# Optimization experiments

Hardware: AMD Instinct MI355X
Metric: run time of the kernel (lower is better)

Reference implementation:

```python
import jax, jax.numpy as jnp
import numpy as np

E, T_MAX, H, L, V = 384, 256, 6, 6, 65
DH = E // H  # 64
EPS = 1e-5


def setup_inputs() -> dict:
    key = jax.random.key(0)
    ks = jax.random.split(key, 24)
    B, T = 128, 256
    s = 0.02
    inp = {
        "input_indices": jax.random.randint(ks[0], (B, T), 0, V, dtype=jnp.int64) if jax.config.read("jax_enable_x64") else jax.random.randint(ks[0], (B, T), 0, V, dtype=jnp.int32),
        "targets": jax.random.randint(ks[1], (B, T), 0, V, dtype=jnp.int32),
        "tok_emb": s * jax.random.normal(ks[2], (V, E), jnp.float32),
        "pos_emb": s * jax.random.normal(ks[3], (T_MAX, E), jnp.float32),
        "Wq": s * jax.random.normal(ks[4], (L, H, E, DH), jnp.float32),
        "Wk": s * jax.random.normal(ks[5], (L, H, E, DH), jnp.float32),
        "Wv": s * jax.random.normal(ks[6], (L, H, E, DH), jnp.float32),
        "Wo": s * jax.random.normal(ks[7], (L, E, E), jnp.float32),
        "bo": jnp.zeros((L, E), jnp.float32),
        "ln1_s": jnp.ones((L, E), jnp.float32),
        "ln1_b": jnp.zeros((L, E), jnp.float32),
        "ln2_s": jnp.ones((L, E), jnp.float32),
        "ln2_b": jnp.zeros((L, E), jnp.float32),
        "W1": s * jax.random.normal(ks[8], (L, E, 4 * E), jnp.float32),
        "b1": jnp.zeros((L, 4 * E), jnp.float32),
        "W2": s * jax.random.normal(ks[9], (L, 4 * E, E), jnp.float32),
        "b2": jnp.zeros((L, E), jnp.float32),
        "lnf_s": jnp.ones((E,), jnp.float32),
        "lnf_b": jnp.zeros((E,), jnp.float32),
        "Wout": s * jax.random.normal(ks[10], (E, V), jnp.float32),
        "bout": jnp.zeros((V,), jnp.float32),
    }
    return inp


def _ln(x, s, b):
    m = x.mean(-1, keepdims=True)
    v = ((x - m) ** 2).mean(-1, keepdims=True)
    return (x - m) * jax.lax.rsqrt(v + EPS) * s + b


def _forward(input_indices, targets, tok_emb, pos_emb, Wq, Wk, Wv, Wo, bo,
             ln1_s, ln1_b, ln2_s, ln2_b, W1, b1, W2, b2, lnf_s, lnf_b, Wout, bout):
    B, T = input_indices.shape
    x = tok_emb[input_indices] + pos_emb[:T]  # [B,T,E]
    causal = jnp.tril(jnp.ones((T, T), bool))
    scale = DH ** -0.5

    def block(x, p):
        wq, wk, wv, wo, bo_, l1s, l1b, l2s, l2b, w1, b1_, w2, b2_ = p
        h = _ln(x, l1s, l1b)
        q = jnp.einsum("bte,hed->bhtd", h, wq)
        k = jnp.einsum("bte,hed->bhtd", h, wk)
        v = jnp.einsum("bte,hed->bhtd", h, wv)
        scores = jnp.einsum("bhtd,bhsd->bhts", q, k) * scale
        scores = jnp.where(causal, scores, -jnp.inf)
        w = jax.nn.softmax(scores, axis=-1)
        att = jnp.einsum("bhts,bhsd->bhtd", w, v)  # [B,H,T,DH]
        att = att.transpose(0, 2, 1, 3).reshape(B, T, E)  # concat heads
        x = x + att @ wo + bo_
        h2 = _ln(x, l2s, l2b)
        ff = jax.nn.relu(h2 @ w1 + b1_) @ w2 + b2_
        return x + ff, None

    x, _ = jax.lax.scan(block, x, (Wq, Wk, Wv, Wo, bo, ln1_s, ln1_b, ln2_s, ln2_b, W1, b1, W2, b2))
    x = _ln(x, lnf_s, lnf_b)
    logits = x @ Wout + bout  # [B,T,V]
    logp = jax.nn.log_softmax(logits, axis=-1)
    nll = -jnp.take_along_axis(logp, targets[..., None], axis=-1)[..., 0]
    loss = nll.mean()
    return logits, loss


def reference(input_indices, targets, tok_emb, pos_emb, Wq, Wk, Wv, Wo, bo,
              ln1_s, ln1_b, ln2_s, ln2_b, W1, b1, W2, b2, lnf_s, lnf_b, Wout, bout):
    return _forward(input_indices, targets, tok_emb, pos_emb, Wq, Wk, Wv, Wo, bo,
                    ln1_s, ln1_b, ln2_s, ln2_b, W1, b1, W2, b2, lnf_s, lnf_b, Wout, bout)
```

## Files before the change

kernel.cpp:

```cpp
#include <hip/hip_runtime.h>

#define BT      32768
#define T_SEQ   256
#define E_DIM   384
#define NH      6
#define NL      6
#define VOC     65
#define FF_DIM  1536
#define QKV_N   1152

typedef short bf16x8 __attribute__((ext_vector_type(8)));
typedef float f32x4  __attribute__((ext_vector_type(4)));
typedef unsigned short u16;

typedef const unsigned int __attribute__((address_space(1))) gu32;
typedef unsigned int       __attribute__((address_space(3))) lu32;

__device__ __forceinline__ u16 f2bf(float x) {
  unsigned u = __builtin_bit_cast(unsigned, x);
  u += 0x7fffu + ((u >> 16) & 1u);
  return (u16)(u >> 16);
}
__device__ __forceinline__ float bf2f(u16 v) {
  unsigned u = ((unsigned)v) << 16;
  return __builtin_bit_cast(float, u);
}

__device__ __forceinline__ void load_lds_16(const void* g, void* l) {
  __builtin_amdgcn_global_load_lds((gu32*)g, (lu32*)l, 16, 0, 0);
}

__global__ __launch_bounds__(256) void transpose_t(
    const float* __restrict__ src, u16* __restrict__ dst, int R, int C,
    long sbs, long dbs_outer, int inner, long dbs_inner, long dbase) {
  __shared__ float t[32][33];
  const int b = blockIdx.z;
  const float* s = src + (long)b * sbs;
  u16* d = dst + dbase + (long)(b / inner) * dbs_outer + (long)(b % inner) * dbs_inner;
  const int r0 = blockIdx.x * 32, c0 = blockIdx.y * 32;
  const int tx = threadIdx.x & 31, ty = threadIdx.x >> 5;
#pragma unroll
  for (int i = 0; i < 4; i++) {
    int rr = ty + i * 8;
    int r = r0 + rr, c = c0 + tx;
    if (r < R && c < C) t[rr][tx] = s[(long)r * C + c];
  }
  __syncthreads();
#pragma unroll
  for (int i = 0; i < 4; i++) {
    int cc = ty + i * 8;
    int c = c0 + cc, r = r0 + tx;
    if (c < C && r < R) d[(long)c * R + r] = f2bf(t[tx][cc]);
  }
}

__global__ __launch_bounds__(256) void embed_k(const int* __restrict__ idx,
                                               const float* __restrict__ tok,
                                               const float* __restrict__ pos,
                                               u16* __restrict__ x) {
  int i = blockIdx.x * 256 + threadIdx.x;
  int bt = i / 48, q = i - bt * 48;
  int t = bt & 255;
  const float4* tp = (const float4*)(tok + (size_t)idx[bt] * E_DIM + q * 8);
  const float4* pp = (const float4*)(pos + (size_t)t * E_DIM + q * 8);
  float4 a0 = tp[0], a1 = tp[1], p0 = pp[0], p1 = pp[1];
  u16 o[8];
  o[0] = f2bf(a0.x + p0.x); o[1] = f2bf(a0.y + p0.y);
  o[2] = f2bf(a0.z + p0.z); o[3] = f2bf(a0.w + p0.w);
  o[4] = f2bf(a1.x + p1.x); o[5] = f2bf(a1.y + p1.y);
  o[6] = f2bf(a1.z + p1.z); o[7] = f2bf(a1.w + p1.w);
  *(bf16x8*)(x + (size_t)bt * E_DIM + q * 8) = *(bf16x8*)o;
}

__global__ __launch_bounds__(256) void ln_k(const u16* __restrict__ x,
                                            const float* __restrict__ gam,
                                            const float* __restrict__ bet,
                                            u16* __restrict__ out) {
  int tid = threadIdx.x, lane = tid & 63, w = tid >> 6;
  size_t token = (size_t)blockIdx.x * 4 + w;
  const u16* xr = x + token * E_DIM;
  u16 raw[6];
  *(uint2*)raw          = *(const uint2*)(xr + 4 * lane);
  *(unsigned*)(raw + 4) = *(const unsigned*)(xr + 256 + 2 * lane);
  float v[6]; float s = 0.f;
#pragma unroll
  for (int i = 0; i < 6; i++) { v[i] = bf2f(raw[i]); s += v[i]; }
#pragma unroll
  for (int d = 1; d < 64; d <<= 1) s += __shfl_xor(s, d);
  float mean = s * (1.f / E_DIM);
  float q = 0.f;
#pragma unroll
  for (int i = 0; i < 6; i++) { float d0 = v[i] - mean; q += d0 * d0; }
#pragma unroll
  for (int d = 1; d < 64; d <<= 1) q += __shfl_xor(q, d);
  float r = rsqrtf(q * (1.f / E_DIM) + 1e-5f);
  int e[6] = {4 * lane, 4 * lane + 1, 4 * lane + 2, 4 * lane + 3,
              256 + 2 * lane, 256 + 2 * lane + 1};
  u16 o[6];
#pragma unroll
  for (int i = 0; i < 6; i++)
    o[i] = f2bf((v[i] - mean) * r * gam[e[i]] + bet[e[i]]);
  u16* orow = out + token * E_DIM;
  *(uint2*)(orow + 4 * lane)          = *(uint2*)o;
  *(unsigned*)(orow + 256 + 2 * lane) = *(unsigned*)(o + 4);
}

__global__ __launch_bounds__(256) void gemm_d(
    const u16* __restrict__ A, const u16* __restrict__ Bt, int K, int Nstore,
    const float* __restrict__ bias, const u16* __restrict__ resid,
    u16* __restrict__ outH, float* __restrict__ outF, int relu) {
  __shared__ u16 smem[16384];
  u16* As = smem;
  u16* Bs = smem + 8192;
  const int tid = threadIdx.x, lane = tid & 63, wv = tid >> 6;
  const int quad = lane >> 4, l16 = lane & 15;
  const int m0 = blockIdx.x * 128, n0 = blockIdx.y * 128;
  const int wm = (wv & 1) * 64, wn = (wv >> 1) * 64;

  const int lrow = lane >> 2;
  const int lchunk = (lane & 3) ^ ((lane >> 3) & 3);

  f32x4 acc[4][4];
#pragma unroll
  for (int i = 0; i < 4; i++)
#pragma unroll
    for (int j = 0; j < 4; j++) acc[i][j] = (f32x4){0.f, 0.f, 0.f, 0.f};

  auto stage = [&](int sel, int k0) {
#pragma unroll
    for (int j = 0; j < 2; j++) {
      int rid = wv * 2 + j;
      int r = rid * 16 + lrow;
      load_lds_16(A + (size_t)(m0 + r) * K + k0 + lchunk * 8, &As[sel * 4096 + rid * 512]);
      load_lds_16(Bt + (size_t)(n0 + r) * K + k0 + lchunk * 8, &Bs[sel * 4096 + rid * 512]);
    }
  };

  const int NK = K >> 5;
  stage(0, 0);
  __syncthreads();
  const int slot = (quad ^ ((l16 >> 1) & 3)) * 8;
  for (int kt = 0; kt < NK; kt++) {
    const int cur = kt & 1;
    if (kt + 1 < NK) stage(cur ^ 1, (kt + 1) * 32);
    const u16* Ab = As + cur * 4096;
    const u16* Bb = Bs + cur * 4096;
    bf16x8 af[4], bfr[4];
#pragma unroll
    for (int i = 0; i < 4; i++) af[i]  = *(const bf16x8*)&Ab[(wm + i * 16 + l16) * 32 + slot];
#pragma unroll
    for (int j = 0; j < 4; j++) bfr[j] = *(const bf16x8*)&Bb[(wn + j * 16 + l16) * 32 + slot];
#pragma unroll
    for (int i = 0; i < 4; i++)
#pragma unroll
      for (int j = 0; j < 4; j++)
        acc[i][j] = __builtin_amdgcn_mfma_f32_16x16x32_bf16(af[i], bfr[j], acc[i][j], 0, 0, 0);
    __syncthreads();
  }

  if (outH) {
#pragma unroll
    for (int p = 0; p < 4; p++) {
      if (p) __syncthreads();
      if ((wv >> 1) == (p >> 1)) {
#pragma unroll
        for (int jj = 0; jj < 2; jj++) {
          int j = (p & 1) * 2 + jj;
          int gn = n0 + wn + j * 16 + l16;
          float bv = bias ? bias[gn] : 0.f;
          int lcol = jj * 16 + l16;
#pragma unroll
          for (int i = 0; i < 4; i++)
#pragma unroll
            for (int r = 0; r < 4; r++) {
              float v = acc[i][j][r] + bv;
              if (relu) v = fmaxf(v, 0.f);
              smem[(wm + i * 16 + quad * 4 + r) * 36 + lcol] = f2bf(v);
            }
        }
      }
      __syncthreads();
      const int gc0 = n0 + p * 32;
#pragma unroll
      for (int s = 0; s < 4; s++) {
        int row = s * 32 + (tid >> 3);
        int seg = (tid & 7) * 4;
        u16 pk[4];
        *(uint2*)pk = *(const uint2*)&smem[row * 36 + seg];
        size_t o = (size_t)(m0 + row) * Nstore + gc0 + seg;
        if (resid) {
          u16 rv[4];
          *(uint2*)rv = *(const uint2*)&resid[o];
#pragma unroll
          for (int q2 = 0; q2 < 4; q2++) pk[q2] = f2bf(bf2f(pk[q2]) + bf2f(rv[q2]));
        }
        *(uint2*)&outH[o] = *(uint2*)pk;
      }
    }
  } else {
#pragma unroll
    for (int j = 0; j < 4; j++) {
      const int gn = n0 + wn + j * 16 + l16;
      if (gn < Nstore) {
        const float bv = bias ? bias[gn] : 0.f;
#pragma unroll
        for (int i = 0; i < 4; i++)
#pragma unroll
          for (int r = 0; r < 4; r++) {
            const int gm = m0 + wm + i * 16 + quad * 4 + r;
            outF[(size_t)gm * Nstore + gn] = acc[i][j][r] + bv;
          }
      }
    }
  }
}

__global__ __launch_bounds__(512) void attn_k(const u16* __restrict__ qkv,
                                              u16* __restrict__ att) {
  __shared__ u16 Kc[64 * 64];
  __shared__ u16 Vtc[64 * 64];
  __shared__ u16 Pl[8 * 16 * 64];
  const int b = blockIdx.x / NH, h = blockIdx.x % NH;
  const int tid = threadIdx.x, lane = tid & 63, w = tid >> 6;
  const int quad = lane >> 4, l16 = lane & 15;
  const int rowb = b * T_SEQ;
  const int tiles[2] = {w, 15 - w};

  bf16x8 qf[2][2];
#pragma unroll
  for (int ti = 0; ti < 2; ti++)
#pragma unroll
    for (int kk = 0; kk < 2; kk++)
      qf[ti][kk] = *(const bf16x8*)(qkv + (size_t)(rowb + tiles[ti] * 16 + l16) * QKV_N +
                                    h * 64 + kk * 32 + quad * 8);

  f32x4 Oa[2][4];
  float mrun[2][4], lrun[2][4];
#pragma unroll
  for (int ti = 0; ti < 2; ti++) {
#pragma unroll
    for (int di = 0; di < 4; di++) Oa[ti][di] = (f32x4){0.f, 0.f, 0.f, 0.f};
#pragma unroll
    for (int r = 0; r < 4; r++) { mrun[ti][r] = -1e30f; lrun[ti][r] = 0.f; }
  }

  u16* Pw = &Pl[w * 1024];
  const int sr = tid >> 3, sseg = tid & 7;
  const int kst = sseg ^ (sr & 7) ^ ((sr >> 3) & 7);

  for (int c = 0; c < 4; c++) {
    const int s0 = c * 64;
    __syncthreads();
    *(uint4*)&Kc[sr * 64 + kst * 8] =
        *(const uint4*)(qkv + (size_t)(rowb + s0 + sr) * QKV_N + 384 + h * 64 + sseg * 8);
    {
      union { uint4 u; u16 us[8]; } tb;
      tb.u = *(const uint4*)(qkv + (size_t)(rowb + s0 + sr) * QKV_N + 768 + h * 64 + sseg * 8);
#pragma unroll
      for (int j = 0; j < 8; j++) {
        int d = sseg * 8 + j;
        int vst = (sr >> 3) ^ (d & 7) ^ ((d >> 3) & 7);
        Vtc[d * 64 + vst * 8 + (sr & 7)] = tb.us[j];
      }
    }
    __syncthreads();

    bf16x8 kf[4][2], vf[4][2];
    bool loaded = false;
#pragma unroll
    for (int ti = 0; ti < 2; ti++) {
      const int t = tiles[ti];
      if (t < 4 * c) continue;
      if (!loaded) {
        loaded = true;
#pragma unroll
        for (int ni = 0; ni < 4; ni++)
#pragma unroll
          for (int kk = 0; kk < 2; kk++) {
            int srow = ni * 16 + l16;
            int ks = (kk * 4 + quad) ^ (srow & 7) ^ ((srow >> 3) & 7);
            kf[ni][kk] = *(const bf16x8*)&Kc[srow * 64 + ks * 8];
            int drow = ni * 16 + l16;
            int vs = (kk * 4 + quad) ^ (drow & 7) ^ ((drow >> 3) & 7);
            vf[ni][kk] = *(const bf16x8*)&Vtc[drow * 64 + vs * 8];
          }
      }
      f32x4 S[4];
#pragma unroll
      for (int ni = 0; ni < 4; ni++) {
        f32x4 z = (f32x4){0.f, 0.f, 0.f, 0.f};
        z = __builtin_amdgcn_mfma_f32_16x16x32_bf16(qf[ti][0], kf[ni][0], z, 0, 0, 0);
        S[ni] = __builtin_amdgcn_mfma_f32_16x16x32_bf16(qf[ti][1], kf[ni][1], z, 0, 0, 0);
      }
      const bool diag = ((t >> 2) == c);
#pragma unroll
      for (int ni = 0; ni < 4; ni++)
#pragma unroll
        for (int r = 0; r < 4; r++) {
          float xv = S[ni][r] * 0.125f;
          if (diag) {
            int trow = t * 16 + quad * 4 + r;
            int s = s0 + ni * 16 + l16;
            if (s > trow) xv = -1e30f;
          }
          S[ni][r] = xv;
        }
#pragma unroll
      for (int r = 0; r < 4; r++) {
        float mx = fmaxf(fmaxf(S[0][r], S[1][r]), fmaxf(S[2][r], S[3][r]));
        mx = fmaxf(mx, __shfl_xor(mx, 1));
        mx = fmaxf(mx, __shfl_xor(mx, 2));
        mx = fmaxf(mx, __shfl_xor(mx, 4));
        mx = fmaxf(mx, __shfl_xor(mx, 8));
        float mnew = fmaxf(mrun[ti][r], mx);
        float alpha = __expf(mrun[ti][r] - mnew);
        float ls = 0.f;
#pragma unroll
        for (int ni = 0; ni < 4; ni++) {
          float p = __expf(S[ni][r] - mnew);
          S[ni][r] = p; ls += p;
        }
        ls += __shfl_xor(ls, 1); ls += __shfl_xor(ls, 2);
        ls += __shfl_xor(ls, 4); ls += __shfl_xor(ls, 8);
        lrun[ti][r] = lrun[ti][r] * alpha + ls;
        mrun[ti][r] = mnew;
#pragma unroll
        for (int di = 0; di < 4; di++) Oa[ti][di][r] *= alpha;
      }
#pragma unroll
      for (int ni = 0; ni < 4; ni++)
#pragma unroll
        for (int r = 0; r < 4; r++) {
          int ch = 2 * ni + (l16 >> 3);
          int st = ch ^ (quad | ((r & 1) << 2));
          Pw[(quad * 4 + r) * 64 + st * 8 + (l16 & 7)] = f2bf(S[ni][r]);
        }
      bf16x8 pf[2];
#pragma unroll
      for (int kk = 0; kk < 2; kk++) {
        int key = (l16 >> 2) | ((l16 & 1) << 2);
        int st = (kk * 4 + quad) ^ key;
        pf[kk] = *(const bf16x8*)&Pw[l16 * 64 + st * 8];
      }
#pragma unroll
      for (int di = 0; di < 4; di++) {
        Oa[ti][di] = __builtin_amdgcn_mfma_f32_16x16x32_bf16(pf[0], vf[di][0], Oa[ti][di], 0, 0, 0);
        Oa[ti][di] = __builtin_amdgcn_mfma_f32_16x16x32_bf16(pf[1], vf[di][1], Oa[ti][di], 0, 0, 0);
      }
    }
  }

#pragma unroll
  for (int ti = 0; ti < 2; ti++)
#pragma unroll
    for (int r = 0; r < 4; r++) {
      float inv = 1.f / lrun[ti][r];
      int trow = tiles[ti] * 16 + quad * 4 + r;
#pragma unroll
      for (int di = 0; di < 4; di++)
        att[(size_t)(rowb + trow) * E_DIM + h * 64 + di * 16 + l16] = f2bf(Oa[ti][di][r] * inv);
    }
}

__global__ __launch_bounds__(256) void loss_k(const float* __restrict__ logits,
                                              const int* __restrict__ tgt,
                                              float* __restrict__ loss) {
  __shared__ float part[4];
  const int tid = threadIdx.x, lane = tid & 63, w = tid >> 6;
  const int wave_id = blockIdx.x * 4 + w;
  float acc = 0.f;
  for (int t = wave_id; t < BT; t += 2048) {
    const float* row = logits + (size_t)t * VOC;
    float a = row[lane];
    float b = (lane == 0) ? row[64] : -1e30f;
    float mx = fmaxf(a, b);
#pragma unroll
    for (int d = 1; d < 64; d <<= 1) mx = fmaxf(mx, __shfl_xor(mx, d));
    float sum = __expf(a - mx) + ((lane == 0) ? __expf(b - mx) : 0.f);
#pragma unroll
    for (int d = 1; d < 64; d <<= 1) sum += __shfl_xor(sum, d);
    if (lane == 0) acc += mx + __logf(sum) - row[tgt[t]];
  }
  if (lane == 0) part[w] = acc;
  __syncthreads();
  if (tid == 0)
    atomicAdd(loss, (part[0] + part[1] + part[2] + part[3]) * (1.f / (float)BT));
}

extern "C" void kernel_launch(void* const* d_in, const int* in_sizes, int n_in,
                              void* d_out, int out_size, void* d_ws, size_t ws_size,
                              hipStream_t stream) {
  (void)in_sizes; (void)n_in; (void)out_size; (void)ws_size;
  const int*   idx  = (const int*)d_in[0];
  const int*   tgt  = (const int*)d_in[1];
  const float* tok  = (const float*)d_in[2];
  const float* pos  = (const float*)d_in[3];
  const float* Wq   = (const float*)d_in[4];
  const float* Wk   = (const float*)d_in[5];
  const float* Wv   = (const float*)d_in[6];
  const float* Wo   = (const float*)d_in[7];
  const float* bo   = (const float*)d_in[8];
  const float* ln1s = (const float*)d_in[9];
  const float* ln1b = (const float*)d_in[10];
  const float* ln2s = (const float*)d_in[11];
  const float* ln2b = (const float*)d_in[12];
  const float* W1   = (const float*)d_in[13];
  const float* b1   = (const float*)d_in[14];
  const float* W2   = (const float*)d_in[15];
  const float* b2   = (const float*)d_in[16];
  const float* lnfs = (const float*)d_in[17];
  const float* lnfb = (const float*)d_in[18];
  const float* Wout = (const float*)d_in[19];
  const float* bout = (const float*)d_in[20];

  char* w = (char*)d_ws;
  u16* x      = (u16*)w;    w += (size_t)BT * E_DIM * 2;
  u16* hb     = (u16*)w;    w += (size_t)BT * E_DIM * 2;
  u16* attb   = (u16*)w;    w += (size_t)BT * E_DIM * 2;
  u16* big    = (u16*)w;    w += (size_t)BT * FF_DIM * 2;
  u16* Wqkv_t = (u16*)w;    w += (size_t)NL * QKV_N * E_DIM * 2;
  u16* Wo_t   = (u16*)w;    w += (size_t)NL * E_DIM * E_DIM * 2;
  u16* W1_t   = (u16*)w;    w += (size_t)NL * FF_DIM * E_DIM * 2;
  u16* W2_t   = (u16*)w;    w += (size_t)NL * E_DIM * FF_DIM * 2;
  u16* Wout_t = (u16*)w;    w += (size_t)128 * E_DIM * 2;
  u16* qkv = big;
  u16* ff  = big;

  float* logits = (float*)d_out;
  float* loss   = logits + (size_t)BT * VOC;

  hipMemsetAsync(Wout_t, 0, 128 * E_DIM * 2, stream);
  transpose_t<<<dim3(12, 2, 36), 256, 0, stream>>>(Wq, Wqkv_t, 384, 64,
      24576, 442368, 6, 24576, 0);
  transpose_t<<<dim3(12, 2, 36), 256, 0, stream>>>(Wk, Wqkv_t, 384, 64,
      24576, 442368, 6, 24576, (long)384 * 384);
  transpose_t<<<dim3(12, 2, 36), 256, 0, stream>>>(Wv, Wqkv_t, 384, 64,
      24576, 442368, 6, 24576, (long)768 * 384);
  transpose_t<<<dim3(12, 12, 6), 256, 0, stream>>>(Wo, Wo_t, 384, 384,
      147456, 147456, 1, 0, 0);
  transpose_t<<<dim3(12, 48, 6), 256, 0, stream>>>(W1, W1_t, 384, 1536,
      589824, 589824, 1, 0, 0);
  transpose_t<<<dim3(48, 12, 6), 256, 0, stream>>>(W2, W2_t, 1536, 384,
      589824, 589824, 1, 0, 0);
  transpose_t<<<dim3(12, 3, 1), 256, 0, stream>>>(Wout, Wout_t, 384, 65,
      0, 0, 1, 0, 0);

  embed_k<<<6144, 256, 0, stream>>>(idx, tok, pos, x);

  for (int l = 0; l < NL; l++) {
    ln_k<<<8192, 256, 0, stream>>>(x, ln1s + l * E_DIM, ln1b + l * E_DIM, hb);
    gemm_d<<<dim3(256, 9), 256, 0, stream>>>(hb, Wqkv_t + (size_t)l * QKV_N * E_DIM,
                                             384, QKV_N, nullptr, nullptr, qkv, nullptr, 0);
    attn_k<<<768, 512, 0, stream>>>(qkv, attb);
    gemm_d<<<dim3(256, 3), 256, 0, stream>>>(attb, Wo_t + (size_t)l * E_DIM * E_DIM,
                                             384, E_DIM, bo + l * E_DIM, x, x, nullptr, 0);
    ln_k<<<8192, 256, 0, stream>>>(x, ln2s + l * E_DIM, ln2b + l * E_DIM, hb);
    gemm_d<<<dim3(256, 12), 256, 0, stream>>>(hb, W1_t + (size_t)l * FF_DIM * E_DIM,
                                              384, FF_DIM, b1 + l * FF_DIM, nullptr, ff, nullptr, 1);
    gemm_d<<<dim3(256, 3), 256, 0, stream>>>(ff, W2_t + (size_t)l * E_DIM * FF_DIM,
                                             1536, E_DIM, b2 + l * E_DIM, x, x, nullptr, 0);
  }
  ln_k<<<8192, 256, 0, stream>>>(x, lnfs, lnfb, hb);
  gemm_d<<<dim3(256, 1), 256, 0, stream>>>(hb, Wout_t, 384, VOC, bout, nullptr, nullptr, logits, 0);

  hipMemsetAsync(loss, 0, 4, stream);
  loss_k<<<512, 256, 0, stream>>>(logits, tgt, loss);
}
```

Before: 1.776 ms.

## Fuse FFN up-projection, ReLU and down-projection into one kernel

```diff
diff --git a/kernel.cpp b/kernel.cpp
--- a/kernel.cpp
+++ b/kernel.cpp
@@ -213,6 +213,128 @@
       }
     }
   }
+}
+
+__global__ __launch_bounds__(512, 2) void ffn_k(
+    const u16* __restrict__ hb, const u16* __restrict__ W1t,
+    const float* __restrict__ b1, const u16* __restrict__ W2t,
+    const float* __restrict__ b2, u16* __restrict__ x) {
+  __shared__ __align__(16) u16 sm[73728];
+  u16* As = sm;
+  u16* Ps = sm + 49152;
+  const int tid = threadIdx.x, lane = tid & 63, w = tid >> 6;
+  const int quad = lane >> 4, l16 = lane & 15;
+  const int wm  = (w >> 2) * 64;
+  const int wn1 = (w & 3) * 48;
+  const int wn2 = (w & 3) * 96;
+  const int m0 = blockIdx.x * 128;
+  const int lrow = lane >> 2;
+  const int lchunk = (lane & 3) ^ ((lane >> 3) & 3);
+  const int slot = (quad ^ ((l16 >> 1) & 3)) * 8;
+
+#pragma unroll
+  for (int p = 0; p < 12; p++)
+    load_lds_16(hb + (size_t)(m0 + w * 16 + lrow) * E_DIM + p * 32 + lchunk * 8,
+                &As[p * 4096 + w * 512]);
+
+  f32x4 oacc[4][6];
+#pragma unroll
+  for (int i = 0; i < 4; i++)
+#pragma unroll
+    for (int o = 0; o < 6; o++) oacc[i][o] = (f32x4){0.f, 0.f, 0.f, 0.f};
+
+  __syncthreads();
+
+  for (int j = 0; j < 8; j++) {
+    const int jb = j * 192;
+    f32x4 pacc[4][3];
+#pragma unroll
+    for (int i = 0; i < 4; i++)
+#pragma unroll
+      for (int f = 0; f < 3; f++) pacc[i][f] = (f32x4){0.f, 0.f, 0.f, 0.f};
+    for (int ks = 0; ks < 12; ks++) {
+      bf16x8 af[4], wf[3];
+#pragma unroll
+      for (int f = 0; f < 3; f++)
+        wf[f] = *(const bf16x8*)(W1t + (size_t)(jb + wn1 + f * 16 + l16) * E_DIM +
+                                 ks * 32 + quad * 8);
+#pragma unroll
+      for (int i = 0; i < 4; i++)
+        af[i] = *(const bf16x8*)&As[ks * 4096 + (wm + i * 16 + l16) * 32 + slot];
+#pragma unroll
+      for (int i = 0; i < 4; i++)
+#pragma unroll
+        for (int f = 0; f < 3; f++)
+          pacc[i][f] = __builtin_amdgcn_mfma_f32_16x16x32_bf16(af[i], wf[f], pacc[i][f], 0, 0, 0);
+    }
+    float bv[3];
+#pragma unroll
+    for (int f = 0; f < 3; f++) bv[f] = b1[jb + wn1 + f * 16 + l16];
+#pragma unroll
+    for (int i = 0; i < 4; i++)
+#pragma unroll
+      for (int f = 0; f < 3; f++) {
+        const int colb = wn1 + f * 16 + l16;
+        const int ch = colb >> 3;
+#pragma unroll
+        for (int r = 0; r < 4; r++) {
+          const int row = wm + i * 16 + quad * 4 + r;
+          Ps[row * 192 + (ch ^ (row & 7)) * 8 + (colb & 7)] =
+              f2bf(fmaxf(pacc[i][f][r] + bv[f], 0.f));
+        }
+      }
+    __syncthreads();
+    for (int ks = 0; ks < 6; ks++) {
+      bf16x8 pf[4], bfr[6];
+#pragma unroll
+      for (int o = 0; o < 6; o++)
+        bfr[o] = *(const bf16x8*)(W2t + (size_t)(wn2 + o * 16 + l16) * FF_DIM +
+                                  jb + ks * 32 + quad * 8);
+#pragma unroll
+      for (int i = 0; i < 4; i++) {
+        const int row = wm + i * 16 + l16;
+        pf[i] = *(const bf16x8*)&Ps[row * 192 + ((ks * 4 + quad) ^ (row & 7)) * 8];
+      }
+#pragma unroll
+      for (int i = 0; i < 4; i++)
+#pragma unroll
+        for (int o = 0; o < 6; o++)
+          oacc[i][o] = __builtin_amdgcn_mfma_f32_16x16x32_bf16(pf[i], bfr[o], oacc[i][o], 0, 0, 0);
+    }
+    __syncthreads();
+  }
+
+  float bv2[6];
+#pragma unroll
+  for (int o = 0; o < 6; o++) bv2[o] = b2[wn2 + o * 16 + l16];
+#pragma unroll
+  for (int i = 0; i < 4; i++)
+#pragma unroll
+    for (int o = 0; o < 6; o++) {
+      const int col = wn2 + o * 16 + l16;
+#pragma unroll
+      for (int r = 0; r < 4; r++) {
+        const int row = wm + i * 16 + quad * 4 + r;
+        sm[row * 392 + col] = f2bf(oacc[i][o][r] + bv2[o]);
+      }
+    }
+  __syncthreads();
+  const int er = tid >> 3, ec = tid & 7;
+#pragma unroll
+  for (int rh = 0; rh < 2; rh++)
+#pragma unroll
+    for (int seg = 0; seg < 6; seg++) {
+      const int row = rh * 64 + er;
+      const int col = (seg * 8 + ec) * 8;
+      u16 pk[8];
+      *(uint4*)pk = *(const uint4*)&sm[row * 392 + col];
+      const size_t g = (size_t)(m0 + row) * E_DIM + col;
+      uint4 rv4 = *(const uint4*)&x[g];
+      const u16* rv = (const u16*)&rv4;
+#pragma unroll
+      for (int q2 = 0; q2 < 8; q2++) pk[q2] = f2bf(bf2f(pk[q2]) + bf2f(rv[q2]));
+      *(uint4*)&x[g] = *(uint4*)pk;
+    }
 }
 
 __global__ __launch_bounds__(512) void attn_k(const u16* __restrict__ qkv,
@@ -424,7 +546,6 @@
   u16* W2_t   = (u16*)w;    w += (size_t)NL * E_DIM * FF_DIM * 2;
   u16* Wout_t = (u16*)w;    w += (size_t)128 * E_DIM * 2;
   u16* qkv = big;
-  u16* ff  = big;
 
   float* logits = (float*)d_out;
   float* loss   = logits + (size_t)BT * VOC;
@@ -455,10 +576,8 @@
     gemm_d<<<dim3(256, 3), 256, 0, stream>>>(attb, Wo_t + (size_t)l * E_DIM * E_DIM,
                                              384, E_DIM, bo + l * E_DIM, x, x, nullptr, 0);
     ln_k<<<8192, 256, 0, stream>>>(x, ln2s + l * E_DIM, ln2b + l * E_DIM, hb);
-    gemm_d<<<dim3(256, 12), 256, 0, stream>>>(hb, W1_t + (size_t)l * FF_DIM * E_DIM,
-                                              384, FF_DIM, b1 + l * FF_DIM, nullptr, ff, nullptr, 1);
-    gemm_d<<<dim3(256, 3), 256, 0, stream>>>(ff, W2_t + (size_t)l * E_DIM * FF_DIM,
-                                             1536, E_DIM, b2 + l * E_DIM, x, x, nullptr, 0);
+    ffn_k<<<256, 512, 0, stream>>>(hb, W1_t + (size_t)l * FF_DIM * E_DIM, b1 + l * FF_DIM,
+                                   W2_t + (size_t)l * E_DIM * FF_DIM, b2 + l * E_DIM, x);
   }
   ln_k<<<8192, 256, 0, stream>>>(x, lnfs, lnfb, hb);
   gemm_d<<<dim3(256, 1), 256, 0, stream>>>(hb, Wout_t, 384, VOC, bout, nullptr, nullptr, logits, 0);
```

After: 2.099 ms. 1.18x slower.
